# Kernel optimization log

Measured on AMD Instinct MI355X. Metric: run time of the kernel, lower is better.

The kernel has to match this reference:

```python
import jax, jax.numpy as jnp
import numpy as np

DEPTH = 16                      # complete binary tree depth (root level = DEPTH)
NUM_LEVELS = DEPTH + 1          # node_order in [0, DEPTH]
N_NODES = 2 ** (DEPTH + 1) - 1  # 131071
VOCAB = 50000
EMB = 128
HID = 128


def setup_inputs() -> dict:
    key = jax.random.key(0)
    ks = jax.random.split(key, 6)
    # --- deterministic complete binary tree structure ---
    idx = np.arange(N_NODES)
    depth = np.floor(np.log2(idx + 1)).astype(np.int64)  # root idx 0 has depth 0
    node_order = (DEPTH - depth).astype(np.int64)        # leaves evaluated first (order 0)
    internal = np.arange(2 ** DEPTH - 1)                 # nodes with children
    parents = np.repeat(internal, 2)                     # consecutive grouping per parent
    children = np.stack([2 * internal + 1, 2 * internal + 2], axis=1).ravel()
    adjacency_list = np.stack([parents, children], axis=1).astype(np.int64)
    edge_order = node_order[parents]
    s = 0.02
    return {
        "features": jax.random.randint(ks[0], (N_NODES,), 0, VOCAB),
        "node_order": jnp.asarray(node_order),
        "adjacency_list": jnp.asarray(adjacency_list),
        "edge_order": jnp.asarray(edge_order),
        "emb": jax.random.normal(ks[1], (VOCAB, EMB), jnp.float32) * s,
        "W_iou": jax.random.normal(ks[2], (EMB, 3 * HID), jnp.float32) * s,
        "b_iou": jnp.zeros((3 * HID,), jnp.float32),
        "U_iou": jax.random.normal(ks[3], (HID, 3 * HID), jnp.float32) * s,
        "W_f": jax.random.normal(ks[4], (EMB, HID), jnp.float32) * s,
        "b_f": jnp.zeros((HID,), jnp.float32),
        "U_f": jax.random.normal(ks[5], (HID, HID), jnp.float32) * s,
    }


def reference(features, node_order, adjacency_list, edge_order,
              emb, W_iou, b_iou, U_iou, W_f, b_f, U_f):
    x = emb[features]                                   # [N, EMB] embedding lookup
    par = adjacency_list[:, 0]                          # [E]
    chd = adjacency_list[:, 1]                          # [E]
    Wx = x @ W_iou + b_iou                              # [N, 3H] input contributions (precomputed)
    Wfx = x @ W_f + b_f                                 # [N, H] forget-gate input term
    N = x.shape[0]
    H = W_f.shape[1]
    h = jnp.zeros((N, H), x.dtype)
    c = jnp.zeros((N, H), x.dtype)
    # level-synchronous TreeLSTM: leaves (level 0) up to root
    for lvl in range(NUM_LEVELS):
        nmask = (node_order == lvl)[:, None]            # nodes updated this level
        emask = (edge_order == lvl)[:, None].astype(x.dtype)  # edges feeding them
        child_h = h[chd]                                # [E, H] gather children
        child_c = c[chd]
        h_sum = jax.ops.segment_sum(child_h * emask, par, num_segments=N)  # [N, H]
        iou = Wx + h_sum @ U_iou                        # [N, 3H]
        i, o, u = jnp.split(iou, 3, axis=1)
        i = jax.nn.sigmoid(i)
        o = jax.nn.sigmoid(o)
        u = jnp.tanh(u)
        f = jax.nn.sigmoid(Wfx[par] + child_h @ U_f)    # [E, H] per-edge forget gate
        c_sum = jax.ops.segment_sum(f * child_c * emask, par, num_segments=N)
        c_new = i * u + c_sum                           # level 0: c_sum == 0 -> i*u (leaf branch)
        c = jnp.where(nmask, c_new, c)
        h = jnp.where(nmask, o * jnp.tanh(c_new), h)
    return h, c
```

## Files before the change

### kernel.cpp

```cpp
#include <hip/hip_runtime.h>
#include <math.h>

#define NN 131071
#define HD 128
#define N_INTERNAL 65535
#define LEAF_BASE 65535

typedef short bf16x8 __attribute__((ext_vector_type(8)));
typedef unsigned short u16x8 __attribute__((ext_vector_type(8)));
typedef unsigned short u16x4 __attribute__((ext_vector_type(4)));
typedef float f32x4 __attribute__((ext_vector_type(4)));

__device__ __forceinline__ float sigm(float z) { return 1.0f / (1.0f + __expf(-z)); }
__device__ __forceinline__ float tanh_f(float z) { return 1.0f - 2.0f / (__expf(2.0f * z) + 1.0f); }

__device__ __forceinline__ unsigned short f2bf(float f) {
    unsigned u = __float_as_uint(f);
    u += 0x7FFFu + ((u >> 16) & 1u);
    return (unsigned short)(u >> 16);
}
__device__ __forceinline__ float bf2f(unsigned short b) {
    return __uint_as_float(((unsigned)b) << 16);
}

__device__ __forceinline__ f32x4 mfma16(bf16x8 a, bf16x8 b, f32x4 c) {
    return __builtin_amdgcn_mfma_f32_16x16x32_bf16(a, b, c, 0, 0, 0);
}

__device__ __forceinline__ float4 addf4(float4 a, float4 b) {
    float4 r; r.x = a.x + b.x; r.y = a.y + b.y; r.z = a.z + b.z; r.w = a.w + b.w; return r;
}

__device__ __forceinline__ bf16x8 pk8(float4 a, float4 b) {
    u16x8 p;
    p[0] = f2bf(a.x); p[1] = f2bf(a.y); p[2] = f2bf(a.z); p[3] = f2bf(a.w);
    p[4] = f2bf(b.x); p[5] = f2bf(b.y); p[6] = f2bf(b.z); p[7] = f2bf(b.w);
    return *(bf16x8*)&p;
}

__device__ __forceinline__ void lds_store8(unsigned short* region, int r, int cc, float4 a, float4 b) {
    u16x8 p;
    p[0] = f2bf(a.x); p[1] = f2bf(a.y); p[2] = f2bf(a.z); p[3] = f2bf(a.w);
    p[4] = f2bf(b.x); p[5] = f2bf(b.y); p[6] = f2bf(b.z); p[7] = f2bf(b.w);
    *(u16x8*)&region[r * HD + ((cc ^ (r & 7)) << 3)] = p;
}

__device__ __forceinline__ bf16x8 lds_frag(const unsigned short* region, int row, int ks, int kl) {
    int cc = ks * 4 + kl;
    return *(const bf16x8*)&region[row * HD + ((cc ^ (row & 7)) << 3)];
}

__device__ __forceinline__ bf16x8 frag2(const unsigned short* M, int ct, int ks, int lane) {
    return *(const bf16x8*)&M[(((ct * 4 + ks) * 64) + lane) * 8];
}

__global__ __launch_bounds__(256) void build_packed(
    const float* __restrict__ W_iou, const float* __restrict__ U_iou,
    const float* __restrict__ W_f, const float* __restrict__ U_f,
    unsigned short* __restrict__ ws)
{
    int f = blockIdx.x * 256 + threadIdx.x;
    int mat = f >> 13;
    int rem = f & 8191;
    int ct = rem >> 8;
    int ks = (rem >> 6) & 3;
    int lane = rem & 63;
    int col = ct * 16 + (lane & 15);
    int k0 = ks * 32 + (lane >> 4) * 8;
    u16x8 out;
#pragma unroll
    for (int e = 0; e < 8; ++e) {
        int k = k0 + e;
        float v;
        if (mat == 0) v = (col < 384) ? W_iou[k * 384 + col] : W_f[k * HD + (col - 384)];
        else          v = (col < 384) ? U_iou[k * 384 + col] : U_f[k * HD + (col - 384)];
        out[e] = f2bf(v);
    }
    *(u16x8*)&ws[(size_t)f * 8] = out;
}

__global__ __launch_bounds__(512) void xp_leaf_kernel(
    const int* __restrict__ feat, const float* __restrict__ emb,
    const unsigned short* __restrict__ WT2,
    const float* __restrict__ b_iou, const float* __restrict__ b_f,
    unsigned short* __restrict__ XPb, float* __restrict__ hbuf, float* __restrict__ cbuf)
{
    __shared__ unsigned short ldsx[64 * HD];
    const int t = threadIdx.x;
    const int m0 = blockIdx.x * 64;
    {
        int r = t >> 3, c8 = t & 7;
        int n = m0 + r;
        int nn = n < NN ? n : 0;
        const float* sx = emb + (size_t)feat[nn] * HD + c8 * 16;
        float4 x0 = *(const float4*)(sx + 0);
        float4 x1 = *(const float4*)(sx + 4);
        float4 x2 = *(const float4*)(sx + 8);
        float4 x3 = *(const float4*)(sx + 12);
        lds_store8(ldsx, r, c8 * 2 + 0, x0, x1);
        lds_store8(ldsx, r, c8 * 2 + 1, x2, x3);
    }
    __syncthreads();

    const int lane = t & 63, w = t >> 6;
    const int jq = w & 3, mh = w >> 2;
    const int l15 = lane & 15, kl = lane >> 4;

    f32x4 zero = {0.f, 0.f, 0.f, 0.f};
    f32x4 acc[4][2][2];
#pragma unroll
    for (int g = 0; g < 4; ++g)
#pragma unroll
        for (int mp = 0; mp < 2; ++mp)
#pragma unroll
            for (int jt = 0; jt < 2; ++jt) acc[g][mp][jt] = zero;

#pragma unroll
    for (int ks = 0; ks < 4; ++ks) {
        bf16x8 a0 = lds_frag(ldsx, (mh * 2 + 0) * 16 + l15, ks, kl);
        bf16x8 a1 = lds_frag(ldsx, (mh * 2 + 1) * 16 + l15, ks, kl);
#pragma unroll
        for (int g = 0; g < 4; ++g) {
#pragma unroll
            for (int jt = 0; jt < 2; ++jt) {
                bf16x8 b = frag2(WT2, g * 8 + jq * 2 + jt, ks, lane);
                acc[g][0][jt] = mfma16(a0, b, acc[g][0][jt]);
                acc[g][1][jt] = mfma16(a1, b, acc[g][1][jt]);
            }
        }
    }

#pragma unroll
    for (int mp = 0; mp < 2; ++mp) {
#pragma unroll
        for (int jt = 0; jt < 2; ++jt) {
            int j = jq * 32 + jt * 16 + l15;
            int nb = m0 + (mh * 2 + mp) * 16 + kl * 4;
            float bi = b_iou[j], bo = b_iou[HD + j], bu = b_iou[2 * HD + j], bf = b_f[j];
#pragma unroll
            for (int r = 0; r < 4; ++r) {
                int n = nb + r;
                if (n >= NN) continue;
                if (n >= LEAF_BASE) {
                    float iv = sigm(acc[0][mp][jt][r] + bi);
                    float ov = sigm(acc[1][mp][jt][r] + bo);
                    float uv = tanh_f(acc[2][mp][jt][r] + bu);
                    float cv = iv * uv;
                    cbuf[(size_t)n * HD + j] = cv;
                    hbuf[(size_t)n * HD + j] = ov * tanh_f(cv);
                } else {
                    u16x4 pk;
                    pk[0] = f2bf(acc[0][mp][jt][r] + bi);
                    pk[1] = f2bf(acc[1][mp][jt][r] + bo);
                    pk[2] = f2bf(acc[2][mp][jt][r] + bu);
                    pk[3] = f2bf(acc[3][mp][jt][r] + bf);
                    *(u16x4*)&XPb[((size_t)n * HD + j) * 4] = pk;
                }
            }
        }
    }
}

__device__ __forceinline__ void level_body(
    unsigned short* lds,
    const unsigned short* __restrict__ UT2, const unsigned short* __restrict__ XPb,
    float* __restrict__ hbuf, float* __restrict__ cbuf, int base, int count, int m0)
{
    unsigned short* ldshs = lds;
    unsigned short* ldsh1 = lds + 8192;
    unsigned short* ldsh2 = lds + 16384;

    const int t = threadIdx.x;
    {
        int r = t >> 3, c8 = t & 7;
        int row = m0 + r;
        int n = base + (row < count ? row : 0);
        const float* s1 = hbuf + (size_t)(2 * n + 1) * HD + c8 * 16;
        const float* s2 = hbuf + (size_t)(2 * n + 2) * HD + c8 * 16;
        float4 p0 = *(const float4*)(s1 + 0);
        float4 p1 = *(const float4*)(s1 + 4);
        float4 p2 = *(const float4*)(s1 + 8);
        float4 p3 = *(const float4*)(s1 + 12);
        float4 q0 = *(const float4*)(s2 + 0);
        float4 q1 = *(const float4*)(s2 + 4);
        float4 q2 = *(const float4*)(s2 + 8);
        float4 q3 = *(const float4*)(s2 + 12);
        lds_store8(ldsh1, r, c8 * 2 + 0, p0, p1);
        lds_store8(ldsh1, r, c8 * 2 + 1, p2, p3);
        lds_store8(ldsh2, r, c8 * 2 + 0, q0, q1);
        lds_store8(ldsh2, r, c8 * 2 + 1, q2, q3);
        lds_store8(ldshs, r, c8 * 2 + 0, addf4(p0, q0), addf4(p1, q1));
        lds_store8(ldshs, r, c8 * 2 + 1, addf4(p2, q2), addf4(p3, q3));
    }
    __syncthreads();

    const int lane = t & 63, w = t >> 6;
    const int jq = w & 3, mh = w >> 2;
    const int l15 = lane & 15, kl = lane >> 4;

    f32x4 zero = {0.f, 0.f, 0.f, 0.f};
    f32x4 acc[5][2][2];
#pragma unroll
    for (int g = 0; g < 5; ++g)
#pragma unroll
        for (int mp = 0; mp < 2; ++mp)
#pragma unroll
            for (int jt = 0; jt < 2; ++jt) acc[g][mp][jt] = zero;

#pragma unroll
    for (int ks = 0; ks < 4; ++ks) {
        bf16x8 ahs0 = lds_frag(ldshs, (mh * 2 + 0) * 16 + l15, ks, kl);
        bf16x8 ahs1 = lds_frag(ldshs, (mh * 2 + 1) * 16 + l15, ks, kl);
        bf16x8 ah10 = lds_frag(ldsh1, (mh * 2 + 0) * 16 + l15, ks, kl);
        bf16x8 ah11 = lds_frag(ldsh1, (mh * 2 + 1) * 16 + l15, ks, kl);
        bf16x8 ah20 = lds_frag(ldsh2, (mh * 2 + 0) * 16 + l15, ks, kl);
        bf16x8 ah21 = lds_frag(ldsh2, (mh * 2 + 1) * 16 + l15, ks, kl);
#pragma unroll
        for (int jt = 0; jt < 2; ++jt) {
            bf16x8 Bi = frag2(UT2,  0 + jq * 2 + jt, ks, lane);
            bf16x8 Bo = frag2(UT2,  8 + jq * 2 + jt, ks, lane);
            bf16x8 Bu = frag2(UT2, 16 + jq * 2 + jt, ks, lane);
            bf16x8 Bf = frag2(UT2, 24 + jq * 2 + jt, ks, lane);
            acc[0][0][jt] = mfma16(ahs0, Bi, acc[0][0][jt]);
            acc[0][1][jt] = mfma16(ahs1, Bi, acc[0][1][jt]);
            acc[1][0][jt] = mfma16(ahs0, Bo, acc[1][0][jt]);
            acc[1][1][jt] = mfma16(ahs1, Bo, acc[1][1][jt]);
            acc[2][0][jt] = mfma16(ahs0, Bu, acc[2][0][jt]);
            acc[2][1][jt] = mfma16(ahs1, Bu, acc[2][1][jt]);
            acc[3][0][jt] = mfma16(ah10, Bf, acc[3][0][jt]);
            acc[3][1][jt] = mfma16(ah11, Bf, acc[3][1][jt]);
            acc[4][0][jt] = mfma16(ah20, Bf, acc[4][0][jt]);
            acc[4][1][jt] = mfma16(ah21, Bf, acc[4][1][jt]);
        }
    }

#pragma unroll
    for (int mp = 0; mp < 2; ++mp) {
#pragma unroll
        for (int jt = 0; jt < 2; ++jt) {
            int j = jq * 32 + jt * 16 + l15;
#pragma unroll
            for (int r = 0; r < 4; ++r) {
                int row = m0 + (mh * 2 + mp) * 16 + kl * 4 + r;
                if (row >= count) continue;
                int n = base + row;
                u16x4 pk = *(const u16x4*)&XPb[((size_t)n * HD + j) * 4];
                float iv = sigm(acc[0][mp][jt][r] + bf2f(pk[0]));
                float ov = sigm(acc[1][mp][jt][r] + bf2f(pk[1]));
                float uv = tanh_f(acc[2][mp][jt][r] + bf2f(pk[2]));
                float fx = bf2f(pk[3]);
                float f1 = sigm(acc[3][mp][jt][r] + fx);
                float f2 = sigm(acc[4][mp][jt][r] + fx);
                float c1 = cbuf[(size_t)(2 * n + 1) * HD + j];
                float c2 = cbuf[(size_t)(2 * n + 2) * HD + j];
                float cn = fmaf(iv, uv, fmaf(f1, c1, f2 * c2));
                cbuf[(size_t)n * HD + j] = cn;
                hbuf[(size_t)n * HD + j] = ov * tanh_f(cn);
            }
        }
    }
}

__global__ __launch_bounds__(512) void level_u_kernel(
    const unsigned short* __restrict__ UT2, const unsigned short* __restrict__ XPb,
    float* __restrict__ hbuf, float* __restrict__ cbuf, int base, int count)
{
    __shared__ unsigned short lds[3 * 64 * HD];
    level_body(lds, UT2, XPb, hbuf, cbuf, base, count, blockIdx.x * 64);
}

__global__ __launch_bounds__(512) void tail_kernel2(
    const unsigned short* __restrict__ UT2, const unsigned short* __restrict__ XPb,
    float* __restrict__ hbuf, float* __restrict__ cbuf)
{
    const int t = threadIdx.x;
    const int lane = t & 63, w = t >> 6;
    const int jq = w & 3, mh = w >> 2;
    const int l15 = lane & 15, kl = lane >> 4;

    for (int lvl = 10; lvl <= 16; ++lvl) {
        const int count = 1 << (16 - lvl);
        const int base = count - 1;
        if (mh * 32 < count) {
            f32x4 zero = {0.f, 0.f, 0.f, 0.f};
            f32x4 acc[5][2][2];
#pragma unroll
            for (int g = 0; g < 5; ++g)
#pragma unroll
                for (int mp = 0; mp < 2; ++mp)
#pragma unroll
                    for (int jt = 0; jt < 2; ++jt) acc[g][mp][jt] = zero;

#pragma unroll
            for (int ks = 0; ks < 4; ++ks) {
                bf16x8 ahs[2], ah1[2], ah2[2];
#pragma unroll
                for (int mp = 0; mp < 2; ++mp) {
                    int row = mh * 32 + mp * 16 + l15;
                    int rr = row < count ? row : count - 1;
                    int n = base + rr;
                    const float* p1 = hbuf + (size_t)(2 * n + 1) * HD + ks * 32 + kl * 8;
                    const float* p2 = hbuf + (size_t)(2 * n + 2) * HD + ks * 32 + kl * 8;
                    float4 a0 = *(const float4*)p1;
                    float4 a1 = *(const float4*)(p1 + 4);
                    float4 b0 = *(const float4*)p2;
                    float4 b1 = *(const float4*)(p2 + 4);
                    ah1[mp] = pk8(a0, a1);
                    ah2[mp] = pk8(b0, b1);
                    ahs[mp] = pk8(addf4(a0, b0), addf4(a1, b1));
                }
#pragma unroll
                for (int jt = 0; jt < 2; ++jt) {
                    bf16x8 Bi = frag2(UT2,  0 + jq * 2 + jt, ks, lane);
                    bf16x8 Bo = frag2(UT2,  8 + jq * 2 + jt, ks, lane);
                    bf16x8 Bu = frag2(UT2, 16 + jq * 2 + jt, ks, lane);
                    bf16x8 Bf = frag2(UT2, 24 + jq * 2 + jt, ks, lane);
                    acc[0][0][jt] = mfma16(ahs[0], Bi, acc[0][0][jt]);
                    acc[0][1][jt] = mfma16(ahs[1], Bi, acc[0][1][jt]);
                    acc[1][0][jt] = mfma16(ahs[0], Bo, acc[1][0][jt]);
                    acc[1][1][jt] = mfma16(ahs[1], Bo, acc[1][1][jt]);
                    acc[2][0][jt] = mfma16(ahs[0], Bu, acc[2][0][jt]);
                    acc[2][1][jt] = mfma16(ahs[1], Bu, acc[2][1][jt]);
                    acc[3][0][jt] = mfma16(ah1[0], Bf, acc[3][0][jt]);
                    acc[3][1][jt] = mfma16(ah1[1], Bf, acc[3][1][jt]);
                    acc[4][0][jt] = mfma16(ah2[0], Bf, acc[4][0][jt]);
                    acc[4][1][jt] = mfma16(ah2[1], Bf, acc[4][1][jt]);
                }
            }

#pragma unroll
            for (int mp = 0; mp < 2; ++mp) {
#pragma unroll
                for (int jt = 0; jt < 2; ++jt) {
                    int j = jq * 32 + jt * 16 + l15;
#pragma unroll
                    for (int r = 0; r < 4; ++r) {
                        int row = mh * 32 + mp * 16 + kl * 4 + r;
                        if (row >= count) continue;
                        int n = base + row;
                        u16x4 pk = *(const u16x4*)&XPb[((size_t)n * HD + j) * 4];
                        float iv = sigm(acc[0][mp][jt][r] + bf2f(pk[0]));
                        float ov = sigm(acc[1][mp][jt][r] + bf2f(pk[1]));
                        float uv = tanh_f(acc[2][mp][jt][r] + bf2f(pk[2]));
                        float fx = bf2f(pk[3]);
                        float f1 = sigm(acc[3][mp][jt][r] + fx);
                        float f2 = sigm(acc[4][mp][jt][r] + fx);
                        float c1 = cbuf[(size_t)(2 * n + 1) * HD + j];
                        float c2 = cbuf[(size_t)(2 * n + 2) * HD + j];
                        float cn = fmaf(iv, uv, fmaf(f1, c1, f2 * c2));
                        cbuf[(size_t)n * HD + j] = cn;
                        hbuf[(size_t)n * HD + j] = ov * tanh_f(cn);
                    }
                }
            }
        }
        __syncthreads();
    }
}

template <int MT>
__global__ __launch_bounds__(128) void leaf_kernel(
    const int* __restrict__ feat, const float* __restrict__ emb,
    const float* __restrict__ W_iou, const float* __restrict__ b_iou,
    float* __restrict__ hbuf, float* __restrict__ cbuf, int base)
{
    __shared__ float X[MT][HD];
    const int j = threadIdx.x;
    const int m0 = blockIdx.x * MT;
#pragma unroll
    for (int m = 0; m < MT; ++m) {
        int n = base + m0 + m;
        X[m][j] = emb[(size_t)feat[n] * HD + j];
    }
    __syncthreads();
    float ai[MT], ao[MT], au[MT];
#pragma unroll
    for (int m = 0; m < MT; ++m) {
        ai[m] = b_iou[j]; ao[m] = b_iou[HD + j]; au[m] = b_iou[2 * HD + j];
    }
#pragma unroll 4
    for (int k = 0; k < HD; ++k) {
        float wi = W_iou[k * 3 * HD + j];
        float wo = W_iou[k * 3 * HD + HD + j];
        float wu = W_iou[k * 3 * HD + 2 * HD + j];
#pragma unroll
        for (int m = 0; m < MT; ++m) {
            float x = X[m][k];
            ai[m] = fmaf(x, wi, ai[m]); ao[m] = fmaf(x, wo, ao[m]); au[m] = fmaf(x, wu, au[m]);
        }
    }
#pragma unroll
    for (int m = 0; m < MT; ++m) {
        int n = base + m0 + m;
        float iv = sigm(ai[m]); float ov = sigm(ao[m]); float uv = tanh_f(au[m]);
        float cv = iv * uv;
        cbuf[(size_t)n * HD + j] = cv;
        hbuf[(size_t)n * HD + j] = ov * tanh_f(cv);
    }
}

template <int MT>
__global__ __launch_bounds__(128) void level_kernel(
    const int* __restrict__ feat, const float* __restrict__ emb,
    const float* __restrict__ W_iou, const float* __restrict__ b_iou,
    const float* __restrict__ U_iou,
    const float* __restrict__ W_f, const float* __restrict__ b_f,
    const float* __restrict__ U_f,
    float* __restrict__ hbuf, float* __restrict__ cbuf, int base)
{
    __shared__ float X[MT][HD];
    __shared__ float H1[MT][HD];
    __shared__ float H2[MT][HD];
    const int j = threadIdx.x;
    const int m0 = blockIdx.x * MT;
#pragma unroll
    for (int m = 0; m < MT; ++m) {
        int n = base + m0 + m;
        X[m][j]  = emb[(size_t)feat[n] * HD + j];
        H1[m][j] = hbuf[(size_t)(2 * n + 1) * HD + j];
        H2[m][j] = hbuf[(size_t)(2 * n + 2) * HD + j];
    }
    __syncthreads();
    float ai[MT], ao[MT], au[MT], g1[MT], g2[MT];
#pragma unroll
    for (int m = 0; m < MT; ++m) {
        ai[m] = b_iou[j]; ao[m] = b_iou[HD + j]; au[m] = b_iou[2 * HD + j];
        g1[m] = b_f[j]; g2[m] = b_f[j];
    }
#pragma unroll 2
    for (int k = 0; k < HD; ++k) {
        float wi = W_iou[k * 3 * HD + j];
        float wo = W_iou[k * 3 * HD + HD + j];
        float wu = W_iou[k * 3 * HD + 2 * HD + j];
        float ui = U_iou[k * 3 * HD + j];
        float uo = U_iou[k * 3 * HD + HD + j];
        float uu = U_iou[k * 3 * HD + 2 * HD + j];
        float wf = W_f[k * HD + j];
        float uf = U_f[k * HD + j];
#pragma unroll
        for (int m = 0; m < MT; ++m) {
            float x = X[m][k]; float h1 = H1[m][k]; float h2 = H2[m][k]; float hs = h1 + h2;
            ai[m] = fmaf(x, wi, fmaf(hs, ui, ai[m]));
            ao[m] = fmaf(x, wo, fmaf(hs, uo, ao[m]));
            au[m] = fmaf(x, wu, fmaf(hs, uu, au[m]));
            g1[m] = fmaf(x, wf, fmaf(h1, uf, g1[m]));
            g2[m] = fmaf(x, wf, fmaf(h2, uf, g2[m]));
        }
    }
#pragma unroll
    for (int m = 0; m < MT; ++m) {
        int n = base + m0 + m;
        float iv = sigm(ai[m]); float ov = sigm(ao[m]); float uv = tanh_f(au[m]);
        float f1 = sigm(g1[m]); float f2 = sigm(g2[m]);
        float c1 = cbuf[(size_t)(2 * n + 1) * HD + j];
        float c2 = cbuf[(size_t)(2 * n + 2) * HD + j];
        float cn = fmaf(iv, uv, fmaf(f1, c1, f2 * c2));
        cbuf[(size_t)n * HD + j] = cn;
        hbuf[(size_t)n * HD + j] = ov * tanh_f(cn);
    }
}

extern "C" void kernel_launch(void* const* d_in, const int* in_sizes, int n_in,
                              void* d_out, int out_size, void* d_ws, size_t ws_size,
                              hipStream_t stream)
{
    const int*   feat  = (const int*)d_in[0];
    const float* emb   = (const float*)d_in[4];
    const float* W_iou = (const float*)d_in[5];
    const float* b_iou = (const float*)d_in[6];
    const float* U_iou = (const float*)d_in[7];
    const float* W_f   = (const float*)d_in[8];
    const float* b_f   = (const float*)d_in[9];
    const float* U_f   = (const float*)d_in[10];

    float* hbuf = (float*)d_out;
    float* cbuf = hbuf + (size_t)NN * HD;

    const size_t PACK_BYTES = 2u * 65536u * 2u;
    const size_t XP_BYTES   = (size_t)N_INTERNAL * HD * 4 * 2;
    if (ws_size >= PACK_BYTES + XP_BYTES) {
        unsigned short* wpk = (unsigned short*)d_ws;
        const unsigned short* WT2 = wpk;
        const unsigned short* UT2 = wpk + 65536;
        unsigned short* XPb = (unsigned short*)((char*)d_ws + PACK_BYTES);

        build_packed<<<64, 256, 0, stream>>>(W_iou, U_iou, W_f, U_f, wpk);
        xp_leaf_kernel<<<2048, 512, 0, stream>>>(feat, emb, WT2, b_iou, b_f, XPb, hbuf, cbuf);

        for (int lvl = 1; lvl <= 9; ++lvl) {
            const int count = 1 << (16 - lvl);
            const int base  = count - 1;
            level_u_kernel<<<count / 64, 512, 0, stream>>>(UT2, XPb, hbuf, cbuf, base, count);
        }
        tail_kernel2<<<1, 512, 0, stream>>>(UT2, XPb, hbuf, cbuf);
    } else {
        leaf_kernel<16><<<65536 / 16, 128, 0, stream>>>(feat, emb, W_iou, b_iou, hbuf, cbuf, 65535);
        for (int lvl = 1; lvl <= 16; ++lvl) {
            const int d = 16 - lvl;
            const int count = 1 << d;
            const int base = count - 1;
            if (count >= 16) {
                level_kernel<16><<<count / 16, 128, 0, stream>>>(
                    feat, emb, W_iou, b_iou, U_iou, W_f, b_f, U_f, hbuf, cbuf, base);
            } else if (count == 8) {
                level_kernel<8><<<1, 128, 0, stream>>>(
                    feat, emb, W_iou, b_iou, U_iou, W_f, b_f, U_f, hbuf, cbuf, base);
            } else if (count == 4) {
                level_kernel<4><<<1, 128, 0, stream>>>(
                    feat, emb, W_iou, b_iou, U_iou, W_f, b_f, U_f, hbuf, cbuf, base);
            } else if (count == 2) {
                level_kernel<2><<<1, 128, 0, stream>>>(
                    feat, emb, W_iou, b_iou, U_iou, W_f, b_f, U_f, hbuf, cbuf, base);
            } else {
                level_kernel<1><<<1, 128, 0, stream>>>(
                    feat, emb, W_iou, b_iou, U_iou, W_f, b_f, U_f, hbuf, cbuf, base);
            }
        }
    }
}
```

Before: 308.8 us.

## Keep tail-level hidden states in LDS as swizzled bf16 for the single-block tail

The single-block tail kernel now stages the level-9 hidden states (nodes 127..254) into shared memory as bf16 with an XOR swizzle, and writes each newly computed h into that buffer as well. Later levels read child fragments from LDS instead of global fp32 memory. The child-sum add moves from an fp32 pre-add into two MFMAs per gate, which doubles the i/o/u MFMA count but drops the fp32 add. The intent is to cut global-memory latency on the serial critical path of the tail. The cost is about 64KB of LDS, extra MFMA work, and slightly different rounding because the children are summed after bf16 conversion.

```diff
diff --git a/kernel.cpp b/kernel.cpp
--- a/kernel.cpp
+++ b/kernel.cpp
@@ -269,15 +269,32 @@
     level_body(lds, UT2, XPb, hbuf, cbuf, base, count, blockIdx.x * 64);
 }
 
-__global__ __launch_bounds__(512) void tail_kernel2(
+__global__ __launch_bounds__(512) void tail_kernel3(
     const unsigned short* __restrict__ UT2, const unsigned short* __restrict__ XPb,
     float* __restrict__ hbuf, float* __restrict__ cbuf)
 {
+    __shared__ unsigned short hlds[255 * HD];
     const int t = threadIdx.x;
+
+    {
+        int n = 127 + (t >> 2);
+        int c0 = (t & 3) * 32;
+        const float* src = hbuf + (size_t)n * HD + c0;
+#pragma unroll
+        for (int q = 0; q < 4; ++q) {
+            float4 a = *(const float4*)(src + q * 8);
+            float4 b = *(const float4*)(src + q * 8 + 4);
+            int cc = (c0 >> 3) + q;
+            *(bf16x8*)&hlds[n * HD + ((cc ^ (n & 7)) << 3)] = pk8(a, b);
+        }
+    }
+    __syncthreads();
+
     const int lane = t & 63, w = t >> 6;
     const int jq = w & 3, mh = w >> 2;
     const int l15 = lane & 15, kl = lane >> 4;
 
+#pragma unroll 1
     for (int lvl = 10; lvl <= 16; ++lvl) {
         const int count = 1 << (16 - lvl);
         const int base = count - 1;
@@ -293,21 +310,14 @@
 
 #pragma unroll
             for (int ks = 0; ks < 4; ++ks) {
-                bf16x8 ahs[2], ah1[2], ah2[2];
+                bf16x8 ah1[2], ah2[2];
 #pragma unroll
                 for (int mp = 0; mp < 2; ++mp) {
                     int row = mh * 32 + mp * 16 + l15;
                     int rr = row < count ? row : count - 1;
                     int n = base + rr;
-                    const float* p1 = hbuf + (size_t)(2 * n + 1) * HD + ks * 32 + kl * 8;
-                    const float* p2 = hbuf + (size_t)(2 * n + 2) * HD + ks * 32 + kl * 8;
-                    float4 a0 = *(const float4*)p1;
-                    float4 a1 = *(const float4*)(p1 + 4);
-                    float4 b0 = *(const float4*)p2;
-                    float4 b1 = *(const float4*)(p2 + 4);
-                    ah1[mp] = pk8(a0, a1);
-                    ah2[mp] = pk8(b0, b1);
-                    ahs[mp] = pk8(addf4(a0, b0), addf4(a1, b1));
+                    ah1[mp] = lds_frag(hlds, 2 * n + 1, ks, kl);
+                    ah2[mp] = lds_frag(hlds, 2 * n + 2, ks, kl);
                 }
 #pragma unroll
                 for (int jt = 0; jt < 2; ++jt) {
@@ -315,16 +325,14 @@
                     bf16x8 Bo = frag2(UT2,  8 + jq * 2 + jt, ks, lane);
                     bf16x8 Bu = frag2(UT2, 16 + jq * 2 + jt, ks, lane);
                     bf16x8 Bf = frag2(UT2, 24 + jq * 2 + jt, ks, lane);
-                    acc[0][0][jt] = mfma16(ahs[0], Bi, acc[0][0][jt]);
-                    acc[0][1][jt] = mfma16(ahs[1], Bi, acc[0][1][jt]);
-                    acc[1][0][jt] = mfma16(ahs[0], Bo, acc[1][0][jt]);
-                    acc[1][1][jt] = mfma16(ahs[1], Bo, acc[1][1][jt]);
-                    acc[2][0][jt] = mfma16(ahs[0], Bu, acc[2][0][jt]);
-                    acc[2][1][jt] = mfma16(ahs[1], Bu, acc[2][1][jt]);
-                    acc[3][0][jt] = mfma16(ah1[0], Bf, acc[3][0][jt]);
-                    acc[3][1][jt] = mfma16(ah1[1], Bf, acc[3][1][jt]);
-                    acc[4][0][jt] = mfma16(ah2[0], Bf, acc[4][0][jt]);
-                    acc[4][1][jt] = mfma16(ah2[1], Bf, acc[4][1][jt]);
+#pragma unroll
+                    for (int mp = 0; mp < 2; ++mp) {
+                        acc[0][mp][jt] = mfma16(ah1[mp], Bi, mfma16(ah2[mp], Bi, acc[0][mp][jt]));
+                        acc[1][mp][jt] = mfma16(ah1[mp], Bo, mfma16(ah2[mp], Bo, acc[1][mp][jt]));
+                        acc[2][mp][jt] = mfma16(ah1[mp], Bu, mfma16(ah2[mp], Bu, acc[2][mp][jt]));
+                        acc[3][mp][jt] = mfma16(ah1[mp], Bf, acc[3][mp][jt]);
+                        acc[4][mp][jt] = mfma16(ah2[mp], Bf, acc[4][mp][jt]);
+                    }
                 }
             }
 
@@ -348,8 +356,11 @@
                         float c1 = cbuf[(size_t)(2 * n + 1) * HD + j];
                         float c2 = cbuf[(size_t)(2 * n + 2) * HD + j];
                         float cn = fmaf(iv, uv, fmaf(f1, c1, f2 * c2));
+                        float hn = ov * tanh_f(cn);
                         cbuf[(size_t)n * HD + j] = cn;
-                        hbuf[(size_t)n * HD + j] = ov * tanh_f(cn);
+                        hbuf[(size_t)n * HD + j] = hn;
+                        int cc = j >> 3;
+                        hlds[n * HD + ((cc ^ (n & 7)) << 3) + (j & 7)] = f2bf(hn);
                     }
                 }
             }
@@ -492,7 +503,7 @@
             const int base  = count - 1;
             level_u_kernel<<<count / 64, 512, 0, stream>>>(UT2, XPb, hbuf, cbuf, base, count);
         }
-        tail_kernel2<<<1, 512, 0, stream>>>(UT2, XPb, hbuf, cbuf);
+        tail_kernel3<<<1, 512, 0, stream>>>(UT2, XPb, hbuf, cbuf);
     } else {
         leaf_kernel<16><<<65536 / 16, 128, 0, stream>>>(feat, emb, W_iou, b_iou, hbuf, cbuf, 65535);
         for (int lvl = 1; lvl <= 16; ++lvl) {
```

New measurement: 290.7 us. 5.9% less time.
